# Kernel tuning notes

Hardware: AMD Instinct MI355X
Metric: run time of the kernel (lower is better)

Reference implementation:

```python
import jax, jax.numpy as jnp
import numpy as np

# par: dt=0.05, tau_m=10.0 -> alpha = 1 - dt/tau_m; v_th = 2.0
ALPHA = 1.0 - 0.05 / 10.0
V_TH = 2.0


def setup_inputs() -> dict:
    key = jax.random.key(0)
    k1, k2 = jax.random.split(key)
    B, T, N = 128, 1000, 1024
    x = jax.random.normal(k1, (B, T, N), dtype=jnp.float32)
    # torch init: normal(mean=0, std=1/sqrt(N))
    w = jax.random.normal(k2, (N,), dtype=jnp.float32) * (1.0 / np.sqrt(N))
    return {"x": x, "w": w}


def reference(x, w):
    """Runs the NeuronClass.__call__ LIF step over all T timesteps.

    v_t = alpha * v_{t-1} + x_t @ w - v_th * stop_grad(z_{t-1})
    z_t = 1[v_t - v_th > 0]
    Returns (v_seq, z_seq), each [B, T].
    """
    B, T, N = x.shape
    # Precompute the input current for all timesteps (same math as per-step x_t @ w,
    # but a single large GEMM instead of T small GEMVs).
    drive = jnp.einsum('btn,n->bt', x, w)  # [B, T]

    def step(carry, i_t):
        v, z = carry
        v = ALPHA * v + i_t - V_TH * jax.lax.stop_gradient(z)
        z = (v - V_TH > 0).astype(v.dtype)
        return (v, z), (v, z)

    v0 = jnp.zeros((B,), dtype=x.dtype)
    z0 = jnp.zeros((B,), dtype=x.dtype)
    _, (v_seq, z_seq) = jax.lax.scan(step, (v0, z0), drive.T)  # scanned outputs [T, B]
    return v_seq.T, z_seq.T
```

## Files before the change

kernel.cpp:

```cpp
#include <hip/hip_runtime.h>


#define ALPHA 0.995f
#define V_TH 2.0f

constexpr int B = 128;
constexpr int T = 1000;
constexpr int N = 1024;

__global__ __launch_bounds__(256) void lif_dot_kernel(
    const float* __restrict__ x, const float* __restrict__ w,
    float* __restrict__ drive_t) {
    const int wave = threadIdx.x >> 6;
    const int lane = threadIdx.x & 63;
    const long long row = (long long)blockIdx.x * 4 + wave;
    const float* xr = x + row * N;

    double acc = 0.0;
#pragma unroll
    for (int it = 0; it < 4; ++it) {
        const int idx = it * 256 + lane * 4;
        const float4 xv = *(const float4*)(xr + idx);
        const float4 wv = *(const float4*)(w + idx);
        acc += (double)xv.x * (double)wv.x;
        acc += (double)xv.y * (double)wv.y;
        acc += (double)xv.z * (double)wv.z;
        acc += (double)xv.w * (double)wv.w;
    }
#pragma unroll
    for (int off = 32; off >= 1; off >>= 1)
        acc += __shfl_down(acc, off);

    if (lane == 0) {
        const int b = (int)(row / T);
        const int t = (int)(row - (long long)b * T);
        drive_t[t * B + b] = (float)acc;
    }
}

__global__ __launch_bounds__(128) void lif_scan_kernel(
    const float* __restrict__ drive_t, float* __restrict__ out) {
    const int b = threadIdx.x;
    float* __restrict__ vout = out + (long long)b * T;
    float* __restrict__ zout = out + (long long)B * T + (long long)b * T;

    float v = 0.0f, z = 0.0f;
    for (int t0 = 0; t0 < T; t0 += 8) {
        float d[8];
#pragma unroll
        for (int j = 0; j < 8; ++j) d[j] = drive_t[(t0 + j) * B + b];
#pragma unroll
        for (int j = 0; j < 8; ++j) {
            v = ALPHA * v + d[j] - V_TH * z;
            z = (v - V_TH > 0.0f) ? 1.0f : 0.0f;
            vout[t0 + j] = v;
            zout[t0 + j] = z;
        }
    }
}

extern "C" void kernel_launch(void* const* d_in, const int* in_sizes, int n_in,
                              void* d_out, int out_size, void* d_ws, size_t ws_size,
                              hipStream_t stream) {
    const float* x = (const float*)d_in[0];
    const float* w = (const float*)d_in[1];
    float* out = (float*)d_out;
    float* drive_t = (float*)d_ws;

    lif_dot_kernel<<<(B * T) / 4, 256, 0, stream>>>(x, w, drive_t);
    lif_scan_kernel<<<1, 128, 0, stream>>>(drive_t, out);
}
```

Measured before the change: 716.1 us.

## Process 16 rows per wave in dot kernel and stage scan outputs through LDS

The dot kernel now has each wave handle 16 rows, two at a time. It keeps w in registers and issues eight independent float4 loads per pair, which raises memory-level parallelism and removes repeated w loads. The scan kernel splits the batch across two blocks and stages drive values and v/z outputs in shared memory per 50-step tile, so global stores become coalesced instead of per-thread strided writes. The cost is more registers per wave, fewer waves in the dot kernel, and extra barriers in the scan.

```diff
diff --git a/kernel.cpp b/kernel.cpp
--- a/kernel.cpp
+++ b/kernel.cpp
@@ -11,50 +11,99 @@
 __global__ __launch_bounds__(256) void lif_dot_kernel(
     const float* __restrict__ x, const float* __restrict__ w,
     float* __restrict__ drive_t) {
-    const int wave = threadIdx.x >> 6;
     const int lane = threadIdx.x & 63;
-    const long long row = (long long)blockIdx.x * 4 + wave;
-    const float* xr = x + row * N;
+    const int gwave = blockIdx.x * 4 + (threadIdx.x >> 6);
+    const int base_row = gwave * 16;
 
-    double acc = 0.0;
+    const float* wp = w + lane * 4;
+    const float4 w0 = *(const float4*)(wp);
+    const float4 w1 = *(const float4*)(wp + 256);
+    const float4 w2 = *(const float4*)(wp + 512);
+    const float4 w3 = *(const float4*)(wp + 768);
+
+    for (int i = 0; i < 16; i += 2) {
+        const float* xr0 = x + (long long)(base_row + i) * N + lane * 4;
+        const float* xr1 = xr0 + N;
+        const float4 a0 = *(const float4*)(xr0);
+        const float4 a1 = *(const float4*)(xr0 + 256);
+        const float4 a2 = *(const float4*)(xr0 + 512);
+        const float4 a3 = *(const float4*)(xr0 + 768);
+        const float4 b0 = *(const float4*)(xr1);
+        const float4 b1 = *(const float4*)(xr1 + 256);
+        const float4 b2 = *(const float4*)(xr1 + 512);
+        const float4 b3 = *(const float4*)(xr1 + 768);
+
+        double s0 = (double)a0.x*w0.x + (double)a0.y*w0.y + (double)a0.z*w0.z + (double)a0.w*w0.w;
+        double s1 = (double)a1.x*w1.x + (double)a1.y*w1.y + (double)a1.z*w1.z + (double)a1.w*w1.w;
+        double s2 = (double)a2.x*w2.x + (double)a2.y*w2.y + (double)a2.z*w2.z + (double)a2.w*w2.w;
+        double s3 = (double)a3.x*w3.x + (double)a3.y*w3.y + (double)a3.z*w3.z + (double)a3.w*w3.w;
+        double t0 = (double)b0.x*w0.x + (double)b0.y*w0.y + (double)b0.z*w0.z + (double)b0.w*w0.w;
+        double t1 = (double)b1.x*w1.x + (double)b1.y*w1.y + (double)b1.z*w1.z + (double)b1.w*w1.w;
+        double t2 = (double)b2.x*w2.x + (double)b2.y*w2.y + (double)b2.z*w2.z + (double)b2.w*w2.w;
+        double t3 = (double)b3.x*w3.x + (double)b3.y*w3.y + (double)b3.z*w3.z + (double)b3.w*w3.w;
+        double accA = (s0 + s1) + (s2 + s3);
+        double accB = (t0 + t1) + (t2 + t3);
+
 #pragma unroll
-    for (int it = 0; it < 4; ++it) {
-        const int idx = it * 256 + lane * 4;
-        const float4 xv = *(const float4*)(xr + idx);
-        const float4 wv = *(const float4*)(w + idx);
-        acc += (double)xv.x * (double)wv.x;
-        acc += (double)xv.y * (double)wv.y;
-        acc += (double)xv.z * (double)wv.z;
-        acc += (double)xv.w * (double)wv.w;
-    }
-#pragma unroll
-    for (int off = 32; off >= 1; off >>= 1)
-        acc += __shfl_down(acc, off);
+        for (int off = 32; off >= 1; off >>= 1) {
+            accA += __shfl_down(accA, off);
+            accB += __shfl_down(accB, off);
+        }
 
-    if (lane == 0) {
-        const int b = (int)(row / T);
-        const int t = (int)(row - (long long)b * T);
-        drive_t[t * B + b] = (float)acc;
+        if (lane == 0) {
+            const int row = base_row + i;
+            const int b = row / T;
+            const int t = row - b * T;
+            drive_t[t * B + b] = (float)accA;
+            const int row2 = row + 1;
+            const int b2 = row2 / T;
+            const int t2 = row2 - b2 * T;
+            drive_t[t2 * B + b2] = (float)accB;
+        }
     }
 }
 
-__global__ __launch_bounds__(128) void lif_scan_kernel(
+__global__ __launch_bounds__(256) void lif_scan_kernel(
     const float* __restrict__ drive_t, float* __restrict__ out) {
-    const int b = threadIdx.x;
-    float* __restrict__ vout = out + (long long)b * T;
-    float* __restrict__ zout = out + (long long)B * T + (long long)b * T;
+    constexpr int TT = 50;
+    constexpr int BB = 64;
+    __shared__ float s_drive[TT][BB];
+    __shared__ float s_v[BB][TT + 1];
+    __shared__ float s_z[BB][TT + 1];
+
+    const int tid = threadIdx.x;
+    const int b0 = blockIdx.x * BB;
+    const int jload = tid >> 6;
+    const int bload = tid & 63;
 
     float v = 0.0f, z = 0.0f;
-    for (int t0 = 0; t0 < T; t0 += 8) {
-        float d[8];
+
+    for (int t0 = 0; t0 < T; t0 += TT) {
+        for (int j = jload; j < TT; j += 4)
+            s_drive[j][bload] = drive_t[(t0 + j) * B + b0 + bload];
+        __syncthreads();
+
+        if (tid < BB) {
 #pragma unroll
-        for (int j = 0; j < 8; ++j) d[j] = drive_t[(t0 + j) * B + b];
-#pragma unroll
-        for (int j = 0; j < 8; ++j) {
-            v = ALPHA * v + d[j] - V_TH * z;
-            z = (v - V_TH > 0.0f) ? 1.0f : 0.0f;
-            vout[t0 + j] = v;
-            zout[t0 + j] = z;
+            for (int j = 0; j < TT; ++j) {
+                const float d = s_drive[j][tid];
+                v = ALPHA * v + d - V_TH * z;
+                z = (v - V_TH > 0.0f) ? 1.0f : 0.0f;
+                s_v[tid][j] = v;
+                s_z[tid][j] = z;
+            }
+        }
+        __syncthreads();
+
+        for (int idx = tid; idx < BB * TT; idx += 256) {
+            const int bb = idx / TT;
+            const int j = idx - bb * TT;
+            out[(long long)(b0 + bb) * T + t0 + j] = s_v[bb][j];
+        }
+        for (int idx = tid; idx < BB * TT; idx += 256) {
+            const int bb = idx / TT;
+            const int j = idx - bb * TT;
+            out[(long long)B * T + (long long)(b0 + bb) * T + t0 + j] = s_z[bb][j];
         }
     }
 }
@@ -67,6 +116,6 @@
     float* out = (float*)d_out;
     float* drive_t = (float*)d_ws;
 
-    lif_dot_kernel<<<(B * T) / 4, 256, 0, stream>>>(x, w, drive_t);
-    lif_scan_kernel<<<1, 128, 0, stream>>>(drive_t, out);
+    lif_dot_kernel<<<2000, 256, 0, stream>>>(x, w, drive_t);
+    lif_scan_kernel<<<2, 256, 0, stream>>>(drive_t, out);
 }
```

Measured after the change: 807.8 us. +12.8%, slower.
